# Kernel tuning notes

Hardware: AMD Instinct MI355X
Metric: run time of the kernel (lower is better)

## Reference

```python
import jax, jax.numpy as jnp
import numpy as np

N_NODES = 100000
N_EDGES = 1600000
D_IN = 128
D_OUT = 128


def setup_inputs() -> dict:
    key = jax.random.key(0)
    k1, k2, k3 = jax.random.split(key, 3)
    x = jax.random.normal(k1, (N_NODES, D_IN), dtype=jnp.float32)
    edge_index = jax.random.randint(k2, (2, N_EDGES), 0, N_NODES, dtype=jnp.int64)
    # Glorot-style init for the GCN weight, zero bias (PyG defaults)
    W = jax.random.normal(k3, (D_IN, D_OUT), dtype=jnp.float32) * (1.0 / np.sqrt(D_IN))
    b = jnp.zeros((D_OUT,), dtype=jnp.float32)
    return {"x": x, "edge_index": edge_index, "W": W, "b": b}


def reference(x, edge_index, W, b):
    # GCNConv (PyG defaults: add_self_loops=True, normalize=True):
    #   out = D^{-1/2} (A + I) D^{-1/2} (X W) + b
    # Dropout is identity in eval mode.
    n = x.shape[0]
    loop = jnp.arange(n, dtype=edge_index.dtype)
    src = jnp.concatenate([edge_index[0], loop])  # [E + N]
    dst = jnp.concatenate([edge_index[1], loop])  # [E + N]

    h = x @ W  # [N, D_OUT] -- transform before aggregation (fewer FLOPs if D_OUT <= D_IN)

    # Degree of each node counting self-loops, computed over targets.
    ones = jnp.ones(dst.shape[0], dtype=h.dtype)
    deg = jax.ops.segment_sum(ones, dst, num_segments=n)  # [N]
    deg_inv_sqrt = jnp.where(deg > 0, jax.lax.rsqrt(deg), 0.0)

    # Symmetric normalization per edge: d_src^{-1/2} * d_dst^{-1/2}
    norm = deg_inv_sqrt[src] * deg_inv_sqrt[dst]  # [E + N]

    # Gather messages, scale, scatter-add to targets.
    msgs = h[src] * norm[:, None]  # [E + N, D_OUT]
    out = jax.ops.segment_sum(msgs, dst, num_segments=n)  # [N, D_OUT]
    return out + b
```

## Files before the change

kernel.cpp:

```cpp
#include <hip/hip_runtime.h>

#define DD 128
#define CAP 12288

typedef __attribute__((ext_vector_type(8))) short bf16x8;
typedef __attribute__((ext_vector_type(4))) float f32x4;

__device__ inline unsigned short f2b(float f) {
    unsigned int u = __float_as_uint(f);
    u += 0x7fffu + ((u >> 16) & 1u);
    return (unsigned short)(u >> 16);
}

__device__ inline void bacc16f(float4& a, float4& b, uint4 v, float s) {
    a.x += __uint_as_float(v.x << 16) * s;
    a.y += __uint_as_float(v.x & 0xffff0000u) * s;
    a.z += __uint_as_float(v.y << 16) * s;
    a.w += __uint_as_float(v.y & 0xffff0000u) * s;
    b.x += __uint_as_float(v.z << 16) * s;
    b.y += __uint_as_float(v.z & 0xffff0000u) * s;
    b.z += __uint_as_float(v.w << 16) * s;
    b.w += __uint_as_float(v.w & 0xffff0000u) * s;
}

__global__ __launch_bounds__(256) void k_pre(const float* __restrict__ W,
                                             unsigned short* __restrict__ Wt,
                                             int* __restrict__ cur, int nbuck) {
    int bid = blockIdx.x;
    if (bid < 64) {
        int idx = bid * 256 + threadIdx.x;
        int k = idx >> 7, c = idx & 127;
        Wt[c * DD + k] = f2b(W[k * DD + c]);
    } else {
        int b = (bid - 64) * 256 + threadIdx.x;
        if (b < nbuck) cur[b] = b * CAP;
    }
}

__global__ __launch_bounds__(256) void k_fA(const int* __restrict__ src,
                                            const int* __restrict__ dst, int E,
                                            int chunk, int nbuck,
                                            int* __restrict__ cur,
                                            int* __restrict__ binned,
                                            const float* __restrict__ x,
                                            const unsigned short* __restrict__ Wt,
                                            unsigned short* __restrict__ hs,
                                            int n, int ngA) {
    const int t = threadIdx.x;
    if ((int)blockIdx.x >= ngA) {
        __shared__ int hist[256];
        __shared__ int base[256];
        __shared__ int curs[256];
        const int e0 = (blockIdx.x - ngA) * chunk;
        const int e1 = min(e0 + chunk, E);

        if (t < 256) { hist[t] = 0; curs[t] = 0; }
        __syncthreads();
        for (int e = e0 + t; e < e1; e += 256)
            atomicAdd(&hist[dst[e] >> 9], 1);
        __syncthreads();
        if (t < nbuck && hist[t] > 0)
            base[t] = atomicAdd(&cur[t], hist[t]);
        __syncthreads();
        for (int e = e0 + t; e < e1; e += 256) {
            int d = dst[e];
            int b = d >> 9;
            int p = atomicAdd(&curs[b], 1);
            int idx = base[b] + p;
            if (idx < (b + 1) * CAP)
                binned[idx] = (src[e] << 9) | (d & 511);
        }
        return;
    }

    const int wave = t >> 6, lane = t & 63;
    const int rowbase = blockIdx.x * 256 + wave * 64;
    const int l15 = lane & 15, l4 = lane >> 4;

    bf16x8 a[4][4];
    #pragma unroll
    for (int rb = 0; rb < 4; ++rb) {
        int r = rowbase + rb * 16 + l15;
        int rc = min(r, n - 1);
        const float* xr = x + (size_t)rc * DD;
        #pragma unroll
        for (int kc = 0; kc < 4; ++kc) {
            int k0 = kc * 32 + l4 * 8;
            float4 f0 = *(const float4*)(xr + k0);
            float4 f1 = *(const float4*)(xr + k0 + 4);
            bf16x8 fr;
            fr[0] = (short)f2b(f0.x); fr[1] = (short)f2b(f0.y);
            fr[2] = (short)f2b(f0.z); fr[3] = (short)f2b(f0.w);
            fr[4] = (short)f2b(f1.x); fr[5] = (short)f2b(f1.y);
            fr[6] = (short)f2b(f1.z); fr[7] = (short)f2b(f1.w);
            a[rb][kc] = fr;
        }
    }

    #pragma unroll
    for (int cb = 0; cb < 8; ++cb) {
        int c0 = cb * 16;
        f32x4 acc[4] = {};
        #pragma unroll
        for (int kc = 0; kc < 4; ++kc) {
            bf16x8 bfrag = *(const bf16x8*)(Wt + (size_t)(c0 + l15) * DD + kc * 32 + l4 * 8);
            #pragma unroll
            for (int rb = 0; rb < 4; ++rb)
                acc[rb] = __builtin_amdgcn_mfma_f32_16x16x32_bf16(a[rb][kc], bfrag, acc[rb], 0, 0, 0);
        }
        #pragma unroll
        for (int rb = 0; rb < 4; ++rb) {
            int r0 = rowbase + rb * 16 + l4 * 4;
            #pragma unroll
            for (int vv = 0; vv < 4; ++vv) {
                int r = r0 + vv;
                if (r < n)
                    hs[(size_t)r * DD + c0 + l15] = f2b(acc[rb][vv]);
            }
        }
    }
}

__global__ __launch_bounds__(512) void k_fB(int* __restrict__ binned,
                                            const int* __restrict__ cur,
                                            int* __restrict__ off,
                                            int* __restrict__ cnt,
                                            float* __restrict__ dinv,
                                            const float* __restrict__ x,
                                            const unsigned short* __restrict__ Wt,
                                            unsigned short* __restrict__ hs,
                                            int n, int nbuck, int growoff) {
    __shared__ int hist[512];
    __shared__ int curs[512];
    __shared__ int sorted[CAP];
    const int t = threadIdx.x;

    if (blockIdx.x < (unsigned)nbuck) {
        const int b = blockIdx.x;
        const int base = b * CAP;
        const int cb = cur[b] - base;

        hist[t] = 0;
        __syncthreads();
        for (int i = t; i < cb; i += 512)
            atomicAdd(&hist[binned[base + i] & 511], 1);
        __syncthreads();
        int v = hist[t];
        for (int st = 1; st < 512; st <<= 1) {
            int tv = (t >= st) ? hist[t - st] : 0;
            __syncthreads();
            hist[t] += tv;
            __syncthreads();
        }
        int excl = hist[t] - v;
        curs[t] = excl;
        int d = b * 512 + t;
        if (d < n) {
            off[d]  = base + excl;
            cnt[d]  = v;
            dinv[d] = rsqrtf((float)v + 1.0f);
        }
        __syncthreads();
        for (int i = t; i < cb; i += 512) {
            int pk = binned[base + i];
            int p = atomicAdd(&curs[pk & 511], 1);
            sorted[p] = pk >> 9;
        }
        __syncthreads();
        for (int i = t; i < cb; i += 512)
            binned[base + i] = sorted[i];
        return;
    }

    const int gb = blockIdx.x - nbuck;
    const int wave = t >> 6, lane = t & 63;
    const int rowbase = growoff + gb * 256 + wave * 32;
    const int l15 = lane & 15, l4 = lane >> 4;

    bf16x8 a[2][4];
    #pragma unroll
    for (int rb = 0; rb < 2; ++rb) {
        int r = rowbase + rb * 16 + l15;
        int rc = min(r, n - 1);
        const float* xr = x + (size_t)rc * DD;
        #pragma unroll
        for (int kc = 0; kc < 4; ++kc) {
            int k0 = kc * 32 + l4 * 8;
            float4 f0 = *(const float4*)(xr + k0);
            float4 f1 = *(const float4*)(xr + k0 + 4);
            bf16x8 fr;
            fr[0] = (short)f2b(f0.x); fr[1] = (short)f2b(f0.y);
            fr[2] = (short)f2b(f0.z); fr[3] = (short)f2b(f0.w);
            fr[4] = (short)f2b(f1.x); fr[5] = (short)f2b(f1.y);
            fr[6] = (short)f2b(f1.z); fr[7] = (short)f2b(f1.w);
            a[rb][kc] = fr;
        }
    }

    #pragma unroll
    for (int cb8 = 0; cb8 < 8; ++cb8) {
        int c0 = cb8 * 16;
        f32x4 acc[2] = {};
        #pragma unroll
        for (int kc = 0; kc < 4; ++kc) {
            bf16x8 bfrag = *(const bf16x8*)(Wt + (size_t)(c0 + l15) * DD + kc * 32 + l4 * 8);
            #pragma unroll
            for (int rb = 0; rb < 2; ++rb)
                acc[rb] = __builtin_amdgcn_mfma_f32_16x16x32_bf16(a[rb][kc], bfrag, acc[rb], 0, 0, 0);
        }
        #pragma unroll
        for (int rb = 0; rb < 2; ++rb) {
            int r0 = rowbase + rb * 16 + l4 * 4;
            #pragma unroll
            for (int vv = 0; vv < 4; ++vv) {
                int r = r0 + vv;
                if (r < n)
                    hs[(size_t)r * DD + c0 + l15] = f2b(acc[rb][vv]);
            }
        }
    }
}

__global__ __launch_bounds__(256, 8) void k_agg(const uint4* __restrict__ hsr,
                                                const int* __restrict__ ssrc,
                                                const int* __restrict__ off,
                                                const int* __restrict__ cnt,
                                                const float* __restrict__ dinv,
                                                const float* __restrict__ bias,
                                                float* __restrict__ out, int n) {
    const int t = threadIdx.x;
    const int wave = t >> 6, lane = t & 63;
    const int q  = lane >> 4;
    const int ql = lane & 15;
    const int d = blockIdx.x * 4 + wave;
    if (d >= n) return;

    const int s0 = off[d];
    const int c  = cnt[d];
    const float di = dinv[d];

    float4 accA = {0.f, 0.f, 0.f, 0.f};
    float4 accB = {0.f, 0.f, 0.f, 0.f};

    uint4 vself = hsr[(size_t)d * 16 + ql];

    int idx[6];
    #pragma unroll
    for (int r = 0; r < 6; ++r) {
        int e = r * 4 + q;
        idx[r] = ssrc[s0 + ((e < c) ? e : 0)];
    }
    #pragma unroll
    for (int r = 0; r < 6; ++r) {
        int e = r * 4 + q;
        idx[r] = (e < c) ? idx[r] : d;
    }

    uint4 val[6];
    float sc[6];
    #pragma unroll
    for (int r = 0; r < 6; ++r) {
        val[r] = hsr[(size_t)idx[r] * 16 + ql];
        sc[r]  = dinv[idx[r]];
    }

    if (q == 0) bacc16f(accA, accB, vself, di);
    #pragma unroll
    for (int r = 0; r < 6; ++r) {
        int e = r * 4 + q;
        if (e < c) bacc16f(accA, accB, val[r], sc[r]);
    }

    for (int i = 24 + q; i < c; i += 4) {
        int s = ssrc[s0 + i];
        uint4 v = hsr[(size_t)s * 16 + ql];
        bacc16f(accA, accB, v, dinv[s]);
    }

    #pragma unroll
    for (int m = 16; m <= 32; m <<= 1) {
        accA.x += __shfl_xor(accA.x, m);
        accA.y += __shfl_xor(accA.y, m);
        accA.z += __shfl_xor(accA.z, m);
        accA.w += __shfl_xor(accA.w, m);
        accB.x += __shfl_xor(accB.x, m);
        accB.y += __shfl_xor(accB.y, m);
        accB.z += __shfl_xor(accB.z, m);
        accB.w += __shfl_xor(accB.w, m);
    }

    if (q == 0) {
        float4 b0 = ((const float4*)bias)[ql * 2];
        float4 b1 = ((const float4*)bias)[ql * 2 + 1];
        float4 o0, o1;
        o0.x = accA.x * di + b0.x;
        o0.y = accA.y * di + b0.y;
        o0.z = accA.z * di + b0.z;
        o0.w = accA.w * di + b0.w;
        o1.x = accB.x * di + b1.x;
        o1.y = accB.y * di + b1.y;
        o1.z = accB.z * di + b1.z;
        o1.w = accB.w * di + b1.w;
        float4* orow = (float4*)(out + (size_t)d * DD);
        orow[ql * 2]     = o0;
        orow[ql * 2 + 1] = o1;
    }
}

extern "C" void kernel_launch(void* const* d_in, const int* in_sizes, int n_in,
                              void* d_out, int out_size, void* d_ws, size_t ws_size,
                              hipStream_t stream) {
    const float* x  = (const float*)d_in[0];
    const int*   ei = (const int*)d_in[1];
    const float* W  = (const float*)d_in[2];
    const float* b  = (const float*)d_in[3];
    float* out = (float*)d_out;

    const int n = in_sizes[0] / DD;
    const int E = in_sizes[1] / 2;
    const int* src = ei;
    const int* dst = ei + E;

    const int nbuck = (n + 511) >> 9;

    unsigned short* hs = (unsigned short*)d_ws;
    unsigned short* Wt = hs + (size_t)n * DD;
    int*   binned = (int*)(Wt + DD * DD);
    int*   off    = binned + (size_t)nbuck * CAP;
    int*   cnt    = off + n;
    float* dinv   = (float*)(cnt + n);
    int*   cur    = (int*)(dinv + n);

    const int nblkA = 256;
    const int chunk = (E + nblkA - 1) / nblkA;

    const int ngA = 195;
    const int growoff = ngA * 256;
    const int ngB = (n - growoff + 255) / 256;

    k_pre<<<64 + (nbuck + 255) / 256, 256, 0, stream>>>(W, Wt, cur, nbuck);
    k_fA <<<ngA + nblkA, 256, 0, stream>>>(src, dst, E, chunk, nbuck, cur, binned,
                                           x, Wt, hs, n, ngA);
    k_fB <<<nbuck + ngB, 512, 0, stream>>>(binned, cur, off, cnt, dinv,
                                           x, Wt, hs, n, nbuck, growoff);
    k_agg<<<(n + 3) / 4, 256, 0, stream>>>((const uint4*)hs, binned, off, cnt,
                                           dinv, b, out, n);
}
```

Before: 124.2 us.

## Split bf16 feature table into two column halves and aggregate per half

The transformed features are now stored as two separate N×64 bf16 tables instead of one N×128 table. The aggregation kernel assigns each node to two blocks, one per column half, interleaved so that groups of blocks work on the same half. Each half-table is 12.8MB rather than 25.6MB, which should fit better in L2/infinite cache during the random gathers. In exchange, the edge indices and dinv values are read twice, and each gathered row segment is 128 bytes instead of 256.

```diff
diff --git a/kernel.cpp b/kernel.cpp
--- a/kernel.cpp
+++ b/kernel.cpp
@@ -12,15 +12,11 @@
     return (unsigned short)(u >> 16);
 }
 
-__device__ inline void bacc16f(float4& a, float4& b, uint4 v, float s) {
+__device__ inline void bacc8f(float4& a, uint2 v, float s) {
     a.x += __uint_as_float(v.x << 16) * s;
     a.y += __uint_as_float(v.x & 0xffff0000u) * s;
     a.z += __uint_as_float(v.y << 16) * s;
     a.w += __uint_as_float(v.y & 0xffff0000u) * s;
-    b.x += __uint_as_float(v.z << 16) * s;
-    b.y += __uint_as_float(v.z & 0xffff0000u) * s;
-    b.z += __uint_as_float(v.w << 16) * s;
-    b.w += __uint_as_float(v.w & 0xffff0000u) * s;
 }
 
 __global__ __launch_bounds__(256) void k_pre(const float* __restrict__ W,
@@ -44,7 +40,8 @@
                                             int* __restrict__ binned,
                                             const float* __restrict__ x,
                                             const unsigned short* __restrict__ Wt,
-                                            unsigned short* __restrict__ hs,
+                                            unsigned short* __restrict__ hs0,
+                                            unsigned short* __restrict__ hs1,
                                             int n, int ngA) {
     const int t = threadIdx.x;
     if ((int)blockIdx.x >= ngA) {
@@ -100,6 +97,8 @@
     #pragma unroll
     for (int cb = 0; cb < 8; ++cb) {
         int c0 = cb * 16;
+        unsigned short* __restrict__ hsd = (cb < 4) ? hs0 : hs1;
+        int lc = (cb & 3) * 16 + l15;
         f32x4 acc[4] = {};
         #pragma unroll
         for (int kc = 0; kc < 4; ++kc) {
@@ -115,7 +114,7 @@
             for (int vv = 0; vv < 4; ++vv) {
                 int r = r0 + vv;
                 if (r < n)
-                    hs[(size_t)r * DD + c0 + l15] = f2b(acc[rb][vv]);
+                    hsd[(size_t)r * 64 + lc] = f2b(acc[rb][vv]);
             }
         }
     }
@@ -128,7 +127,8 @@
                                             float* __restrict__ dinv,
                                             const float* __restrict__ x,
                                             const unsigned short* __restrict__ Wt,
-                                            unsigned short* __restrict__ hs,
+                                            unsigned short* __restrict__ hs0,
+                                            unsigned short* __restrict__ hs1,
                                             int n, int nbuck, int growoff) {
     __shared__ int hist[512];
     __shared__ int curs[512];
@@ -200,6 +200,8 @@
     #pragma unroll
     for (int cb8 = 0; cb8 < 8; ++cb8) {
         int c0 = cb8 * 16;
+        unsigned short* __restrict__ hsd = (cb8 < 4) ? hs0 : hs1;
+        int lc = (cb8 & 3) * 16 + l15;
         f32x4 acc[2] = {};
         #pragma unroll
         for (int kc = 0; kc < 4; ++kc) {
@@ -215,13 +217,14 @@
             for (int vv = 0; vv < 4; ++vv) {
                 int r = r0 + vv;
                 if (r < n)
-                    hs[(size_t)r * DD + c0 + l15] = f2b(acc[rb][vv]);
+                    hsd[(size_t)r * 64 + lc] = f2b(acc[rb][vv]);
             }
         }
     }
 }
 
-__global__ __launch_bounds__(256, 8) void k_agg(const uint4* __restrict__ hsr,
+__global__ __launch_bounds__(256, 8) void k_agg(const uint2* __restrict__ hs0,
+                                                const uint2* __restrict__ hs1,
                                                 const int* __restrict__ ssrc,
                                                 const int* __restrict__ off,
                                                 const int* __restrict__ cnt,
@@ -232,17 +235,19 @@
     const int wave = t >> 6, lane = t & 63;
     const int q  = lane >> 4;
     const int ql = lane & 15;
-    const int d = blockIdx.x * 4 + wave;
+    const int g = blockIdx.x >> 3, r8 = blockIdx.x & 7;
+    const int half = r8 >> 2, sub = r8 & 3;
+    const int d = (g * 4 + sub) * 4 + wave;
     if (d >= n) return;
+    const uint2* __restrict__ hsr = half ? hs1 : hs0;
 
     const int s0 = off[d];
     const int c  = cnt[d];
     const float di = dinv[d];
 
-    float4 accA = {0.f, 0.f, 0.f, 0.f};
-    float4 accB = {0.f, 0.f, 0.f, 0.f};
-
-    uint4 vself = hsr[(size_t)d * 16 + ql];
+    float4 acc = {0.f, 0.f, 0.f, 0.f};
+
+    uint2 vself = hsr[(size_t)d * 16 + ql];
 
     int idx[6];
     #pragma unroll
@@ -256,7 +261,7 @@
         idx[r] = (e < c) ? idx[r] : d;
     }
 
-    uint4 val[6];
+    uint2 val[6];
     float sc[6];
     #pragma unroll
     for (int r = 0; r < 6; ++r) {
@@ -264,46 +269,35 @@
         sc[r]  = dinv[idx[r]];
     }
 
-    if (q == 0) bacc16f(accA, accB, vself, di);
+    if (q == 0) bacc8f(acc, vself, di);
     #pragma unroll
     for (int r = 0; r < 6; ++r) {
         int e = r * 4 + q;
-        if (e < c) bacc16f(accA, accB, val[r], sc[r]);
+        if (e < c) bacc8f(acc, val[r], sc[r]);
     }
 
     for (int i = 24 + q; i < c; i += 4) {
         int s = ssrc[s0 + i];
-        uint4 v = hsr[(size_t)s * 16 + ql];
-        bacc16f(accA, accB, v, dinv[s]);
+        uint2 v = hsr[(size_t)s * 16 + ql];
+        bacc8f(acc, v, dinv[s]);
     }
 
     #pragma unroll
     for (int m = 16; m <= 32; m <<= 1) {
-        accA.x += __shfl_xor(accA.x, m);
-        accA.y += __shfl_xor(accA.y, m);
-        accA.z += __shfl_xor(accA.z, m);
-        accA.w += __shfl_xor(accA.w, m);
-        accB.x += __shfl_xor(accB.x, m);
-        accB.y += __shfl_xor(accB.y, m);
-        accB.z += __shfl_xor(accB.z, m);
-        accB.w += __shfl_xor(accB.w, m);
+        acc.x += __shfl_xor(acc.x, m);
+        acc.y += __shfl_xor(acc.y, m);
+        acc.z += __shfl_xor(acc.z, m);
+        acc.w += __shfl_xor(acc.w, m);
     }
 
     if (q == 0) {
-        float4 b0 = ((const float4*)bias)[ql * 2];
-        float4 b1 = ((const float4*)bias)[ql * 2 + 1];
-        float4 o0, o1;
-        o0.x = accA.x * di + b0.x;
-        o0.y = accA.y * di + b0.y;
-        o0.z = accA.z * di + b0.z;
-        o0.w = accA.w * di + b0.w;
-        o1.x = accB.x * di + b1.x;
-        o1.y = accB.y * di + b1.y;
-        o1.z = accB.z * di + b1.z;
-        o1.w = accB.w * di + b1.w;
-        float4* orow = (float4*)(out + (size_t)d * DD);
-        orow[ql * 2]     = o0;
-        orow[ql * 2 + 1] = o1;
+        float4 bb = ((const float4*)bias)[half * 16 + ql];
+        float4 o;
+        o.x = acc.x * di + bb.x;
+        o.y = acc.y * di + bb.y;
+        o.z = acc.z * di + bb.z;
+        o.w = acc.w * di + bb.w;
+        ((float4*)(out + (size_t)d * DD + half * 64))[ql] = o;
     }
 }
 
@@ -323,8 +317,9 @@
 
     const int nbuck = (n + 511) >> 9;
 
-    unsigned short* hs = (unsigned short*)d_ws;
-    unsigned short* Wt = hs + (size_t)n * DD;
+    unsigned short* hs0 = (unsigned short*)d_ws;
+    unsigned short* hs1 = hs0 + (size_t)n * 64;
+    unsigned short* Wt  = hs1 + (size_t)n * 64;
     int*   binned = (int*)(Wt + DD * DD);
     int*   off    = binned + (size_t)nbuck * CAP;
     int*   cnt    = off + n;
@@ -338,11 +333,14 @@
     const int growoff = ngA * 256;
     const int ngB = (n - growoff + 255) / 256;
 
+    const int nodeblk = (n + 3) / 4;
+    const int gcnt = (nodeblk + 3) / 4;
+
     k_pre<<<64 + (nbuck + 255) / 256, 256, 0, stream>>>(W, Wt, cur, nbuck);
     k_fA <<<ngA + nblkA, 256, 0, stream>>>(src, dst, E, chunk, nbuck, cur, binned,
-                                           x, Wt, hs, n, ngA);
+                                           x, Wt, hs0, hs1, n, ngA);
     k_fB <<<nbuck + ngB, 512, 0, stream>>>(binned, cur, off, cnt, dinv,
-                                           x, Wt, hs, n, nbuck, growoff);
-    k_agg<<<(n + 3) / 4, 256, 0, stream>>>((const uint4*)hs, binned, off, cnt,
-                                           dinv, b, out, n);
-}
+                                           x, Wt, hs0, hs1, n, nbuck, growoff);
+    k_agg<<<gcnt * 8, 256, 0, stream>>>((const uint2*)hs0, (const uint2*)hs1,
+                                        binned, off, cnt, dinv, b, out, n);
+}
```

Measured after the change: 140.5 us. 13.1% more time.
